# Optimization experiments

Hardware: AMD Instinct MI355X
Metric: run time of the kernel (lower is better)

Reference implementation:

```python
import jax, jax.numpy as jnp
import numpy as np

N = 4096            # data_length
T_IN, D_IN = 64, 128
F = 32 * 64         # target_length * output_dim


def setup_inputs() -> dict:
    key = jax.random.key(0)
    k1, k2, k3, k4 = jax.random.split(key, 4)
    xs = jax.random.normal(k1, (N, T_IN, D_IN), dtype=jnp.float32)
    W = jax.random.normal(k2, (T_IN * D_IN, F), dtype=jnp.float32) / np.sqrt(T_IN * D_IN)
    ys = jax.random.randint(k3, (N,), 0, 2, dtype=jnp.int32)  # {0,1} -> mapped to +-1 labels
    alphas = jax.random.normal(k4, (N,), dtype=jnp.float32)
    return {"xs": xs, "W": W, "ys": ys, "alphas": alphas}


def reference(xs, W, ys, alphas):
    gamma = 1.0 / F  # RBF bandwidth
    # encoder (stand-in for seq2seq): [N, T*D] @ [T*D, F] -> [N, F]
    X = xs.reshape(N, -1) @ W
    # pairwise squared distances via gram trick
    sq = jnp.sum(X * X, axis=-1)                       # [N]
    d2 = sq[:, None] + sq[None, :] - 2.0 * (X @ X.T)   # [N, N]
    d2 = jnp.maximum(d2, 0.0)
    K = jnp.exp(-gamma * d2)                           # RBF kernel matrix
    lab = (2 * ys - 1).astype(X.dtype)                 # +-1 labels
    G = (lab[:, None] * lab[None, :]) * K              # gram[i][j] = y_i y_j k(x_i, x_j)
    # 0.5 * alpha^T G alpha - sum(alpha)
    value = 0.5 * jnp.dot(alphas, G @ alphas) - jnp.sum(alphas)
    return value.reshape(1, 1)
```

## Files before the change

kernel.cpp:

```cpp
#include <hip/hip_runtime.h>
#include <hip/hip_bf16.h>

#define N_ROWS 4096
#define K_IN   8192
#define F_DIM  2048
#define GAMMA  (1.0f / 2048.0f)

typedef unsigned short u16;
typedef unsigned int   u32;
typedef unsigned char  u8;
typedef __attribute__((ext_vector_type(4))) int   i32x4;
typedef __attribute__((ext_vector_type(8))) int   i32x8;
typedef __attribute__((ext_vector_type(4))) float f32x4;
typedef __attribute__((ext_vector_type(2))) float f32x2;


__device__ __forceinline__ u32 pk4_fp8(float a, float b, float c, float d) {
  u32 u = 0;
  u = __builtin_amdgcn_cvt_pk_fp8_f32(a, b, u, false);
  u = __builtin_amdgcn_cvt_pk_fp8_f32(c, d, u, true);
  return u;
}
__device__ __forceinline__ u8 f8(float v) {
  return (u8)(__builtin_amdgcn_cvt_pk_fp8_f32(v, v, 0, false) & 0xff);
}

__device__ __forceinline__ void async16(const void* g, void* l) {
  __builtin_amdgcn_global_load_lds(
      (const __attribute__((address_space(1))) void*)g,
      (__attribute__((address_space(3))) void*)l, 16, 0, 0);
}


__global__ void convert_xs(const float* __restrict__ xs, u8* __restrict__ out) {
  __shared__ float t16[16][132];
  const int bid = blockIdx.x;
  const int rt = bid >> 6, kt = bid & 63;
  const int tid = threadIdx.x;
  const float* src = xs + (size_t)rt * 16 * K_IN + kt * 128;
#pragma unroll
  for (int j = 0; j < 2; ++j) {
    int i = tid + j * 256;
    int row = i >> 5, c4 = (i & 31) << 2;
    float4 v = *(const float4*)(src + (size_t)row * K_IN + c4);
    t16[row][c4 + 0] = v.x; t16[row][c4 + 1] = v.y;
    t16[row][c4 + 2] = v.z; t16[row][c4 + 3] = v.w;
  }
  __syncthreads();
  const int cw = tid >> 1, part = tid & 1;
  const int h = cw >> 6, l = cw & 63, q = l >> 4, rr = l & 15;
  const float* p = &t16[rr][q * 32 + h * 16 + part * 8];
  u32 u0 = pk4_fp8(p[0], p[1], p[2], p[3]);
  u32 u1 = pk4_fp8(p[4], p[5], p[6], p[7]);
  uint2 st = {u0, u1};
  *(uint2*)(out + ((size_t)(rt * 64 + kt) << 11) + cw * 16 + part * 8) = st;
}

__global__ void transpose_w(const float* __restrict__ W, u8* __restrict__ Wt) {
  __shared__ float tile[128][33];
  int k0 = blockIdx.x * 128;
  int f0 = blockIdx.y * 32;
  int tx = threadIdx.x, ty = threadIdx.y;
#pragma unroll
  for (int kk = 0; kk < 16; ++kk) {
    int k = kk * 8 + ty;
    tile[k][tx] = 64.0f * W[(size_t)(k0 + k) * F_DIM + f0 + tx];
  }
  __syncthreads();
  const int kt = k0 >> 7;
#pragma unroll
  for (int ff = 0; ff < 4; ++ff) {
    int f = ff * 8 + ty;
    int kk = tx * 4;
    u32 p = pk4_fp8(tile[kk][f], tile[kk + 1][f], tile[kk + 2][f], tile[kk + 3][f]);
    int rt = (f0 + f) >> 4, rr = (f0 + f) & 15;
    int q = kk >> 5, hh = (kk >> 4) & 1, b = kk & 15;
    *(u32*)(Wt + ((size_t)(rt * 64 + kt) << 11) + hh * 1024 + (q * 16 + rr) * 16 + b) = p;
  }
}

__global__ void prep(const float* __restrict__ alphas, const int* __restrict__ ys,
                     float* __restrict__ beta, float* __restrict__ out) {
  __shared__ float red[1024];
  int t = threadIdx.x;
  float s = 0.f;
  for (int i = t; i < N_ROWS; i += 1024) {
    float a = alphas[i];
    beta[i] = a * (float)(2 * ys[i] - 1);
    s += a;
  }
  red[t] = s;
  __syncthreads();
  for (int off = 512; off; off >>= 1) {
    if (t < off) red[t] += red[t + off];
    __syncthreads();
  }
  if (t == 0) out[0] = -red[0];
}

__global__ void row_sq(const u32* __restrict__ X, float* __restrict__ sq) {
  int wave = threadIdx.x >> 6, lane = threadIdx.x & 63;
  int row = blockIdx.x * 4 + wave;
  const u8* base = (const u8*)X + ((size_t)(row >> 4) << 15);
  const int rr = row & 15;
  float s = 0.f;
#pragma unroll
  for (int it = 0; it < 2; ++it) {
    int c = lane + it * 64;
    int kt = c >> 3, q = (c >> 1) & 3, h = c & 1;
    uint4 v = *(const uint4*)(base + kt * 2048 + h * 1024 + (q * 16 + rr) * 16);
    u32 w[4] = {v.x, v.y, v.z, v.w};
#pragma unroll
    for (int p = 0; p < 4; ++p) {
      f32x2 lo = __builtin_amdgcn_cvt_pk_f32_fp8(w[p], false);
      f32x2 hi = __builtin_amdgcn_cvt_pk_f32_fp8(w[p], true);
      s += lo[0] * lo[0] + lo[1] * lo[1] + hi[0] * hi[0] + hi[1] * hi[1];
    }
  }
#pragma unroll
  for (int off = 32; off; off >>= 1) s += __shfl_down(s, off);
  if (lane == 0) sq[row] = s;
}

__global__ __launch_bounds__(512, 2) void gemm_xw(const u8* __restrict__ A,
                                                  const u8* __restrict__ Bt,
                                                  u8* __restrict__ X) {
  __shared__ __align__(16) u8 smem[131072];
  const int tid = threadIdx.x;
  const int wg = blockIdx.x;
  const int L = (wg & 7) * 32 + (wg >> 3);
  const int m0 = (L & 15) << 8;
  const int n0 = (L >> 4) << 7;

  const int lane = tid & 63;
  const int wave = tid >> 6;
  const int kh = wave >> 2;
  const int w2 = wave & 3;
  const int wm = (w2 >> 1) << 7;
  const int wn = (w2 & 1) << 6;
  const int t = tid & 255;

  u8* sA  = smem + kh * 65536;
  u8* sB0 = sA + 32768;
  u8* sB1 = sB0 + 16384;

  const u8* pA = A  + (size_t)((m0 >> 4) + (t >> 7)) * 131072 + (t & 127) * 16;
  const u8* pB = Bt + (size_t)((n0 >> 4) + (t >> 7)) * 131072 + (t & 127) * 16;
  const int oT = t * 16;

  f32x4 acc[8][4];
  const f32x4 zero = {0.f, 0.f, 0.f, 0.f};
#pragma unroll
  for (int i = 0; i < 8; ++i)
#pragma unroll
    for (int j = 0; j < 4; ++j) acc[i][j] = zero;

#define STAGE_A(KT) { _Pragma("unroll") for (int j_ = 0; j_ < 8; ++j_) \
    async16(pA + (size_t)j_ * 262144 + (size_t)(KT) * 2048, sA + oT + j_ * 4096); }
#define STAGE_B(BUF, KT) { _Pragma("unroll") for (int j_ = 0; j_ < 4; ++j_) \
    async16(pB + (size_t)j_ * 262144 + (size_t)(KT) * 2048, (BUF) + oT + j_ * 4096); }
#define MFMA1(MT, NT, AF, BG) \
    acc[MT][NT] = __builtin_amdgcn_mfma_scale_f32_16x16x128_f8f6f4( \
        AF, BG, acc[MT][NT], 0, 0, 0, 127, 0, 121);

  const int kbase = kh * 32;
  STAGE_A(kbase)
  STAGE_B(sB0, kbase)
  __syncthreads();

  const int aB = lane * 16;
  const int sa0 = wm >> 4;
  const int sb0i = wn >> 4;

  for (int it = 0; it < 32; ++it) {
    const int kt = kbase + it;
    u8* sBc = (it & 1) ? sB1 : sB0;
    u8* sBn = (it & 1) ? sB0 : sB1;

    i32x8 af[8];
#pragma unroll
    for (int mt = 0; mt < 8; ++mt) {
      const u8* b_ = sA + (sa0 + mt) * 2048 + aB;
      i32x4 lo = *(const i32x4*)(b_);
      i32x4 hi = *(const i32x4*)(b_ + 1024);
      af[mt] = (i32x8){lo[0], lo[1], lo[2], lo[3], hi[0], hi[1], hi[2], hi[3]};
    }
    __syncthreads();

    if (it < 31) { STAGE_A(kt + 1) STAGE_B(sBn, kt + 1) }
#pragma unroll
    for (int nt = 0; nt < 4; ++nt) {
      const u8* b_ = sBc + (sb0i + nt) * 2048 + aB;
      i32x4 lo = *(const i32x4*)(b_);
      i32x4 hi = *(const i32x4*)(b_ + 1024);
      i32x8 bg = (i32x8){lo[0], lo[1], lo[2], lo[3], hi[0], hi[1], hi[2], hi[3]};
      MFMA1(0, nt, af[0], bg) MFMA1(1, nt, af[1], bg)
      MFMA1(2, nt, af[2], bg) MFMA1(3, nt, af[3], bg)
      MFMA1(4, nt, af[4], bg) MFMA1(5, nt, af[5], bg)
      MFMA1(6, nt, af[6], bg) MFMA1(7, nt, af[7], bg)
    }
    __syncthreads();
  }
#undef STAGE_A
#undef STAGE_B
#undef MFMA1

  __syncthreads();
  float* red = (float*)smem;
  if (kh == 1) {
#pragma unroll
    for (int mt = 0; mt < 8; ++mt)
#pragma unroll
      for (int nt = 0; nt < 4; ++nt)
        *(f32x4*)(red + ((size_t)t * 32 + mt * 4 + nt) * 4) = acc[mt][nt];
  }
  __syncthreads();
  if (kh == 0) {
    const int q = lane >> 4, r = lane & 15;
    const int qq0 = wn >> 5;
#pragma unroll
    for (int mt = 0; mt < 8; ++mt) {
#pragma unroll
      for (int nt = 0; nt < 4; ++nt) {
        f32x4 v = acc[mt][nt] + *(const f32x4*)(red + ((size_t)t * 32 + mt * 4 + nt) * 4);
        const int rt = (m0 >> 4) + (wm >> 4) + mt;
        const int qq = qq0 + (nt >> 1);
        const int hh = nt & 1;
        u8* dst = X + (size_t)rt * 32768 + (size_t)(n0 >> 7) * 2048 + hh * 1024 + r;
#pragma unroll
        for (int e = 0; e < 4; ++e)
          dst[(qq * 16 + ((q << 2) + e)) * 16] = f8(v[e]);
      }
    }
  }
}

__device__ __forceinline__ void gemm_tile_x(const u8* __restrict__ X, int m0, int n0,
                                            u8* sA, u8* sB, int tid, f32x4 acc[4][4]) {
  const int lane = tid & 63;
  const int wave = tid >> 6;
  const f32x4 zero = {0.f, 0.f, 0.f, 0.f};
#pragma unroll
  for (int mt = 0; mt < 4; ++mt)
#pragma unroll
    for (int nt = 0; nt < 4; ++nt) acc[mt][nt] = zero;

  const u8* pA = X + (size_t)((m0 >> 4) + (tid >> 7)) * 32768 + (tid & 127) * 16;
  const u8* pB = X + (size_t)((n0 >> 4) + (tid >> 7)) * 32768 + (tid & 127) * 16;
  const int oT = tid * 16;
  const int aB = lane * 16;
  const int sa0 = (wave >> 1) * 4, sb0 = (wave & 1) * 4;

  for (int kt = 0; kt < 16; ++kt) {
#pragma unroll
    for (int j = 0; j < 4; ++j) {
      async16(pA + (size_t)j * 65536 + kt * 2048, sA + oT + j * 4096);
      async16(pB + (size_t)j * 65536 + kt * 2048, sB + oT + j * 4096);
    }
    __syncthreads();

    i32x8 af[4], bg[4];
#pragma unroll
    for (int mt = 0; mt < 4; ++mt) {
      const u8* b_ = sA + (sa0 + mt) * 2048 + aB;
      i32x4 lo = *(const i32x4*)(b_);
      i32x4 hi = *(const i32x4*)(b_ + 1024);
      af[mt] = (i32x8){lo[0], lo[1], lo[2], lo[3], hi[0], hi[1], hi[2], hi[3]};
    }
#pragma unroll
    for (int nt = 0; nt < 4; ++nt) {
      const u8* b_ = sB + (sb0 + nt) * 2048 + aB;
      i32x4 lo = *(const i32x4*)(b_);
      i32x4 hi = *(const i32x4*)(b_ + 1024);
      bg[nt] = (i32x8){lo[0], lo[1], lo[2], lo[3], hi[0], hi[1], hi[2], hi[3]};
    }
#pragma unroll
    for (int mt = 0; mt < 4; ++mt)
#pragma unroll
      for (int nt = 0; nt < 4; ++nt)
        acc[mt][nt] = __builtin_amdgcn_mfma_scale_f32_16x16x128_f8f6f4(
            af[mt], bg[nt], acc[mt][nt], 0, 0, 0, 127, 0, 127);
    __syncthreads();
  }
}

__global__ __launch_bounds__(256, 3) void gemm_kern(const u8* __restrict__ X,
                                                    const float* __restrict__ sq,
                                                    const float* __restrict__ beta,
                                                    float* __restrict__ out) {
  __shared__ __align__(16) u8 sA[128 * 128];
  __shared__ __align__(16) u8 sB[128 * 128];
  const int tid = threadIdx.x;
  int bid = blockIdx.x;
  int ib = 0;
  while (bid >= 32 - ib) { bid -= 32 - ib; ++ib; }
  const int jb = ib + bid;
  const int m0 = ib << 7;
  const int n0 = jb << 7;

  f32x4 acc[4][4];
  gemm_tile_x(X, m0, n0, sA, sB, tid, acc);

  const int lane = tid & 63;
  const int q = lane >> 4;
  const int r = lane & 15;
  const int wave = tid >> 6;
  const int wm = (wave >> 1) << 6;
  const int wn = (wave & 1) << 6;

  float sqj[4], bj[4];
#pragma unroll
  for (int nt = 0; nt < 4; ++nt) {
    int j = n0 + wn + (nt << 4) + r;
    sqj[nt] = sq[j];
    bj[nt] = beta[j];
  }
  float local = 0.f;
#pragma unroll
  for (int mt = 0; mt < 4; ++mt) {
#pragma unroll
    for (int e = 0; e < 4; ++e) {
      int i = m0 + wm + (mt << 4) + (q << 2) + e;
      float sqi = sq[i];
      float bi = beta[i];
#pragma unroll
      for (int nt = 0; nt < 4; ++nt) {
        float d2 = fmaxf(sqi + sqj[nt] - 2.f * acc[mt][nt][e], 0.f);
        local += bi * bj[nt] * __expf(-GAMMA * d2);
      }
    }
  }
  local *= (ib == jb) ? 0.5f : 1.0f;
#pragma unroll
  for (int off = 32; off; off >>= 1) local += __shfl_down(local, off);
  if (lane == 0) atomicAdd(out, local);
}


extern "C" void kernel_launch(void* const* d_in, const int* in_sizes, int n_in,
                              void* d_out, int out_size, void* d_ws, size_t ws_size,
                              hipStream_t stream) {
  const float* xs = (const float*)d_in[0];
  const float* W = (const float*)d_in[1];
  const int* ys = (const int*)d_in[2];
  const float* alphas = (const float*)d_in[3];
  float* out = (float*)d_out;

  char* ws = (char*)d_ws;
  u8* xs_f8 = (u8*)ws;
  u8* Wt_f8 = (u8*)(ws + 33554432);
  u8* X_f8  = (u8*)(ws + 50331648);
  float* sq   = (float*)(ws + 58720256);
  float* beta = (float*)(ws + 58736640);

  convert_xs<<<16384, 256, 0, stream>>>(xs, xs_f8);
  dim3 tb(32, 8);
  dim3 tg(K_IN / 128, F_DIM / 32);
  transpose_w<<<tg, tb, 0, stream>>>(W, Wt_f8);
  prep<<<1, 1024, 0, stream>>>(alphas, ys, beta, out);

  gemm_xw<<<256, 512, 0, stream>>>(xs_f8, Wt_f8, X_f8);
  row_sq<<<N_ROWS / 4, 256, 0, stream>>>((const u32*)X_f8, sq);
  gemm_kern<<<528, 256, 0, stream>>>(X_f8, sq, beta, out);
}
```

Baseline: 358.8 us.

## Double-buffer Gram GEMM, fuse row norms into XW epilogue, coalesce W transpose stores

The Gram-matrix GEMM now double-buffers its LDS tiles, prefetching the next K tile while the current one computes. Its occupancy hint drops from 3 to 2 blocks per CU to make room for the extra LDS. Row squared norms are computed in the XW GEMM epilogue from the fp8-quantized values and added with atomics, which removes the separate row_sq kernel; prep now zeroes sq first. transpose_w stages its fp8 output in LDS so it can write 16-byte coalesced stores, and s_setprio raises wave priority around the MFMA sections. Together these target load latency, one kernel launch and scattered global stores, at the cost of fewer resident blocks and atomic contention.

```diff
diff --git a/kernel.cpp b/kernel.cpp
--- a/kernel.cpp
+++ b/kernel.cpp
@@ -21,9 +21,6 @@
   u = __builtin_amdgcn_cvt_pk_fp8_f32(c, d, u, true);
   return u;
 }
-__device__ __forceinline__ u8 f8(float v) {
-  return (u8)(__builtin_amdgcn_cvt_pk_fp8_f32(v, v, 0, false) & 0xff);
-}
 
 __device__ __forceinline__ void async16(const void* g, void* l) {
   __builtin_amdgcn_global_load_lds(
@@ -58,6 +55,7 @@
 
 __global__ void transpose_w(const float* __restrict__ W, u8* __restrict__ Wt) {
   __shared__ float tile[128][33];
+  __shared__ u32 ob[1024];
   int k0 = blockIdx.x * 128;
   int f0 = blockIdx.y * 32;
   int tx = threadIdx.x, ty = threadIdx.y;
@@ -67,26 +65,32 @@
     tile[k][tx] = 64.0f * W[(size_t)(k0 + k) * F_DIM + f0 + tx];
   }
   __syncthreads();
-  const int kt = k0 >> 7;
 #pragma unroll
   for (int ff = 0; ff < 4; ++ff) {
     int f = ff * 8 + ty;
     int kk = tx * 4;
     u32 p = pk4_fp8(tile[kk][f], tile[kk + 1][f], tile[kk + 2][f], tile[kk + 3][f]);
-    int rt = (f0 + f) >> 4, rr = (f0 + f) & 15;
-    int q = kk >> 5, hh = (kk >> 4) & 1, b = kk & 15;
-    *(u32*)(Wt + ((size_t)(rt * 64 + kt) << 11) + hh * 1024 + (q * 16 + rr) * 16 + b) = p;
-  }
+    int rtl = f >> 4, rr = f & 15;
+    int q = kk >> 5, hh = (kk >> 4) & 1;
+    ob[rtl * 512 + hh * 256 + (q * 16 + rr) * 4 + ((kk & 15) >> 2)] = p;
+  }
+  __syncthreads();
+  const int t = ty * 32 + tx;
+  const int kt = k0 >> 7, rt0 = f0 >> 4;
+  uint4* dst = (uint4*)(Wt + ((size_t)((rt0 + (t >> 7)) * 64 + kt) << 11));
+  dst[t & 127] = ((const uint4*)ob)[t];
 }
 
 __global__ void prep(const float* __restrict__ alphas, const int* __restrict__ ys,
-                     float* __restrict__ beta, float* __restrict__ out) {
+                     float* __restrict__ beta, float* __restrict__ sq,
+                     float* __restrict__ out) {
   __shared__ float red[1024];
   int t = threadIdx.x;
   float s = 0.f;
   for (int i = t; i < N_ROWS; i += 1024) {
     float a = alphas[i];
     beta[i] = a * (float)(2 * ys[i] - 1);
+    sq[i] = 0.f;
     s += a;
   }
   red[t] = s;
@@ -98,33 +102,10 @@
   if (t == 0) out[0] = -red[0];
 }
 
-__global__ void row_sq(const u32* __restrict__ X, float* __restrict__ sq) {
-  int wave = threadIdx.x >> 6, lane = threadIdx.x & 63;
-  int row = blockIdx.x * 4 + wave;
-  const u8* base = (const u8*)X + ((size_t)(row >> 4) << 15);
-  const int rr = row & 15;
-  float s = 0.f;
-#pragma unroll
-  for (int it = 0; it < 2; ++it) {
-    int c = lane + it * 64;
-    int kt = c >> 3, q = (c >> 1) & 3, h = c & 1;
-    uint4 v = *(const uint4*)(base + kt * 2048 + h * 1024 + (q * 16 + rr) * 16);
-    u32 w[4] = {v.x, v.y, v.z, v.w};
-#pragma unroll
-    for (int p = 0; p < 4; ++p) {
-      f32x2 lo = __builtin_amdgcn_cvt_pk_f32_fp8(w[p], false);
-      f32x2 hi = __builtin_amdgcn_cvt_pk_f32_fp8(w[p], true);
-      s += lo[0] * lo[0] + lo[1] * lo[1] + hi[0] * hi[0] + hi[1] * hi[1];
-    }
-  }
-#pragma unroll
-  for (int off = 32; off; off >>= 1) s += __shfl_down(s, off);
-  if (lane == 0) sq[row] = s;
-}
-
 __global__ __launch_bounds__(512, 2) void gemm_xw(const u8* __restrict__ A,
                                                   const u8* __restrict__ Bt,
-                                                  u8* __restrict__ X) {
+                                                  u8* __restrict__ X,
+                                                  float* __restrict__ sqp) {
   __shared__ __align__(16) u8 smem[131072];
   const int tid = threadIdx.x;
   const int wg = blockIdx.x;
@@ -188,6 +169,7 @@
     __syncthreads();
 
     if (it < 31) { STAGE_A(kt + 1) STAGE_B(sBn, kt + 1) }
+    __builtin_amdgcn_s_setprio(1);
 #pragma unroll
     for (int nt = 0; nt < 4; ++nt) {
       const u8* b_ = sBc + (sb0i + nt) * 2048 + aB;
@@ -199,6 +181,7 @@
       MFMA1(4, nt, af[4], bg) MFMA1(5, nt, af[5], bg)
       MFMA1(6, nt, af[6], bg) MFMA1(7, nt, af[7], bg)
     }
+    __builtin_amdgcn_s_setprio(0);
     __syncthreads();
   }
 #undef STAGE_A
@@ -220,23 +203,38 @@
     const int qq0 = wn >> 5;
 #pragma unroll
     for (int mt = 0; mt < 8; ++mt) {
+      float rs[4] = {0.f, 0.f, 0.f, 0.f};
 #pragma unroll
       for (int nt = 0; nt < 4; ++nt) {
         f32x4 v = acc[mt][nt] + *(const f32x4*)(red + ((size_t)t * 32 + mt * 4 + nt) * 4);
+        u32 pk = pk4_fp8(v[0], v[1], v[2], v[3]);
+        f32x2 lo = __builtin_amdgcn_cvt_pk_f32_fp8(pk, false);
+        f32x2 hi = __builtin_amdgcn_cvt_pk_f32_fp8(pk, true);
+        rs[0] += lo[0] * lo[0]; rs[1] += lo[1] * lo[1];
+        rs[2] += hi[0] * hi[0]; rs[3] += hi[1] * hi[1];
         const int rt = (m0 >> 4) + (wm >> 4) + mt;
         const int qq = qq0 + (nt >> 1);
         const int hh = nt & 1;
         u8* dst = X + (size_t)rt * 32768 + (size_t)(n0 >> 7) * 2048 + hh * 1024 + r;
-#pragma unroll
-        for (int e = 0; e < 4; ++e)
-          dst[(qq * 16 + ((q << 2) + e)) * 16] = f8(v[e]);
+        dst[(qq * 16 + ((q << 2) + 0)) * 16] = (u8)(pk & 0xff);
+        dst[(qq * 16 + ((q << 2) + 1)) * 16] = (u8)((pk >> 8) & 0xff);
+        dst[(qq * 16 + ((q << 2) + 2)) * 16] = (u8)((pk >> 16) & 0xff);
+        dst[(qq * 16 + ((q << 2) + 3)) * 16] = (u8)(pk >> 24);
       }
+#pragma unroll
+      for (int e = 0; e < 4; ++e) {
+        float s = rs[e];
+        s += __shfl_xor(s, 1); s += __shfl_xor(s, 2);
+        s += __shfl_xor(s, 4); s += __shfl_xor(s, 8);
+        if (r == 0) atomicAdd(sqp + m0 + wm + (mt << 4) + (q << 2) + e, s);
+      }
     }
   }
 }
 
 __device__ __forceinline__ void gemm_tile_x(const u8* __restrict__ X, int m0, int n0,
-                                            u8* sA, u8* sB, int tid, f32x4 acc[4][4]) {
+                                            u8 (*sA)[16384], u8 (*sB)[16384],
+                                            int tid, f32x4 acc[4][4]) {
   const int lane = tid & 63;
   const int wave = tid >> 6;
   const f32x4 zero = {0.f, 0.f, 0.f, 0.f};
@@ -251,45 +249,51 @@
   const int aB = lane * 16;
   const int sa0 = (wave >> 1) * 4, sb0 = (wave & 1) * 4;
 
+#define STG(KT, BUF) { _Pragma("unroll") for (int j_ = 0; j_ < 4; ++j_) { \
+    async16(pA + (size_t)j_ * 65536 + (size_t)(KT) * 2048, sA[BUF] + oT + j_ * 4096); \
+    async16(pB + (size_t)j_ * 65536 + (size_t)(KT) * 2048, sB[BUF] + oT + j_ * 4096); } }
+
+  STG(0, 0)
+  __syncthreads();
+
   for (int kt = 0; kt < 16; ++kt) {
-#pragma unroll
-    for (int j = 0; j < 4; ++j) {
-      async16(pA + (size_t)j * 65536 + kt * 2048, sA + oT + j * 4096);
-      async16(pB + (size_t)j * 65536 + kt * 2048, sB + oT + j * 4096);
-    }
-    __syncthreads();
+    const int cur = kt & 1, nxt = cur ^ 1;
+    if (kt < 15) STG(kt + 1, nxt)
 
     i32x8 af[4], bg[4];
 #pragma unroll
     for (int mt = 0; mt < 4; ++mt) {
-      const u8* b_ = sA + (sa0 + mt) * 2048 + aB;
+      const u8* b_ = sA[cur] + (sa0 + mt) * 2048 + aB;
       i32x4 lo = *(const i32x4*)(b_);
       i32x4 hi = *(const i32x4*)(b_ + 1024);
       af[mt] = (i32x8){lo[0], lo[1], lo[2], lo[3], hi[0], hi[1], hi[2], hi[3]};
     }
 #pragma unroll
     for (int nt = 0; nt < 4; ++nt) {
-      const u8* b_ = sB + (sb0 + nt) * 2048 + aB;
+      const u8* b_ = sB[cur] + (sb0 + nt) * 2048 + aB;
       i32x4 lo = *(const i32x4*)(b_);
       i32x4 hi = *(const i32x4*)(b_ + 1024);
       bg[nt] = (i32x8){lo[0], lo[1], lo[2], lo[3], hi[0], hi[1], hi[2], hi[3]};
     }
+    __builtin_amdgcn_s_setprio(1);
 #pragma unroll
     for (int mt = 0; mt < 4; ++mt)
 #pragma unroll
       for (int nt = 0; nt < 4; ++nt)
         acc[mt][nt] = __builtin_amdgcn_mfma_scale_f32_16x16x128_f8f6f4(
             af[mt], bg[nt], acc[mt][nt], 0, 0, 0, 127, 0, 127);
+    __builtin_amdgcn_s_setprio(0);
     __syncthreads();
   }
-}
-
-__global__ __launch_bounds__(256, 3) void gemm_kern(const u8* __restrict__ X,
+#undef STG
+}
+
+__global__ __launch_bounds__(256, 2) void gemm_kern(const u8* __restrict__ X,
                                                     const float* __restrict__ sq,
                                                     const float* __restrict__ beta,
                                                     float* __restrict__ out) {
-  __shared__ __align__(16) u8 sA[128 * 128];
-  __shared__ __align__(16) u8 sB[128 * 128];
+  __shared__ __align__(16) u8 sA[2][16384];
+  __shared__ __align__(16) u8 sB[2][16384];
   const int tid = threadIdx.x;
   int bid = blockIdx.x;
   int ib = 0;
@@ -357,9 +361,8 @@
   dim3 tb(32, 8);
   dim3 tg(K_IN / 128, F_DIM / 32);
   transpose_w<<<tg, tb, 0, stream>>>(W, Wt_f8);
-  prep<<<1, 1024, 0, stream>>>(alphas, ys, beta, out);
-
-  gemm_xw<<<256, 512, 0, stream>>>(xs_f8, Wt_f8, X_f8);
-  row_sq<<<N_ROWS / 4, 256, 0, stream>>>((const u32*)X_f8, sq);
+  prep<<<1, 1024, 0, stream>>>(alphas, ys, beta, sq, out);
+
+  gemm_xw<<<256, 512, 0, stream>>>(xs_f8, Wt_f8, X_f8, sq);
   gemm_kern<<<528, 256, 0, stream>>>(X_f8, sq, beta, out);
 }
```

Result: no change. 364.5 us (+1.6%).
